# Optimization experiments

Measured on AMD Instinct MI355X. Metric: run time of the kernel, lower is better.

## Reference

```python
import jax, jax.numpy as jnp
import numpy as np

N_NODES = 50000
N_EDGES = 1600000
N_FEAT = 512
N_HID = 128
N_CLASSES = 2
NUM_GRAPHS = 128


def setup_inputs() -> dict:
    key = jax.random.key(0)
    k_x, k_e, k_w1, k_b1, k_w2, k_b2 = jax.random.split(key, 6)
    x = jax.random.normal(k_x, (N_NODES, N_FEAT), dtype=jnp.float32)
    edge_index = jax.random.randint(k_e, (2, N_EDGES), 0, N_NODES, dtype=jnp.int64)
    # evenly spaced graph ids -> every graph segment non-empty for max pool
    batch = (jnp.arange(N_NODES, dtype=jnp.int64) * NUM_GRAPHS) // N_NODES
    # GCNConv weight (glorot-ish) and bias; lin2 head
    W1 = jax.random.normal(k_w1, (N_FEAT, N_HID), dtype=jnp.float32) * (1.0 / np.sqrt(N_FEAT))
    b1 = jnp.zeros((N_HID,), dtype=jnp.float32)
    W2 = jax.random.normal(k_w2, (N_HID, N_CLASSES), dtype=jnp.float32) * (1.0 / np.sqrt(N_HID))
    b2 = jnp.zeros((N_CLASSES,), dtype=jnp.float32)
    return {"x": x, "W1": W1, "b1": b1, "W2": W2, "b2": b2,
            "edge_index": edge_index, "batch": batch}


def _gcn_conv(x, edge_index, W, b):
    # PyG GCNConv: add self loops, symmetric norm, aggregate src->dst
    src, dst = edge_index[0], edge_index[1]
    loops = jnp.arange(N_NODES, dtype=src.dtype)
    src = jnp.concatenate([src, loops])
    dst = jnp.concatenate([dst, loops])
    deg = jax.ops.segment_sum(jnp.ones_like(dst, dtype=x.dtype), dst,
                              num_segments=N_NODES)
    dinv = jnp.where(deg > 0, jax.lax.rsqrt(deg), 0.0)
    norm = dinv[src] * dinv[dst]                      # [E+N]
    h = x @ W                                         # [N, nhid]
    msgs = h[src] * norm[:, None]                     # gather + scale
    out = jax.ops.segment_sum(msgs, dst, num_segments=N_NODES)
    return out + b


def reference(x, W1, b1, W2, b2, edge_index, batch):
    h = jax.nn.relu(_gcn_conv(x, edge_index, W1, b1))       # [N, nhid]
    pooled = jax.ops.segment_max(h, batch, num_segments=NUM_GRAPHS)  # [G, nhid]
    logits = pooled @ W2 + b2                               # [G, num_classes]
    return jax.nn.log_softmax(logits, axis=-1)
```

## Files before the change

kernel.cpp:

```cpp
#include <hip/hip_runtime.h>

#define N_NODES   50000
#define N_EDGES   1600000
#define N_FEAT    512
#define N_HID     128
#define NUM_GRAPHS 128
#define N_WAVES_GEMM 3125
#define PREP_DINV_BLOCKS 196

#define CAP          96
#define NSLICE       8
#define SLICE_NODES  6250
#define NCHUNK       128
#define CHUNK_E      12500

typedef short bf16x8 __attribute__((ext_vector_type(8)));
typedef float f32x4  __attribute__((ext_vector_type(4)));

static __device__ __forceinline__ unsigned short f2bf(float f) {
  union { float f; unsigned int u; } v; v.f = f;
  unsigned int u = v.u;
  unsigned int r = (u + 0x7FFFu + ((u >> 16) & 1u)) >> 16;
  return (unsigned short)r;
}
static __device__ __forceinline__ float bfl(unsigned int w) {
  union { unsigned int u; float f; } v; v.u = w << 16; return v.f;
}
static __device__ __forceinline__ float bfh(unsigned int w) {
  union { unsigned int u; float f; } v; v.u = w & 0xFFFF0000u; return v.f;
}

__global__ void init_ws(int* __restrict__ cnt, int* __restrict__ pooled) {
  int i = blockIdx.x * 256 + threadIdx.x;
  if (i < N_NODES) cnt[i] = 0;
  if (i < NUM_GRAPHS * N_HID) pooled[i] = 0;
}

__global__ __launch_bounds__(256) void scatter_slice(const int* __restrict__ edge,
                                                     int* __restrict__ cnt,
                                                     unsigned short* __restrict__ sedge) {
  const int chunk = blockIdx.x >> 3;
  const int lo = (blockIdx.x & 7) * SLICE_NODES;
  const int e0 = chunk * CHUNK_E;
  for (int e = e0 + threadIdx.x; e < e0 + CHUNK_E; e += 256) {
    int d = edge[N_EDGES + e];
    if ((unsigned)(d - lo) < (unsigned)SLICE_NODES) {
      int s = edge[e];
      int pos = atomicAdd(&cnt[d], 1);
      if (pos < CAP) sedge[(size_t)d * CAP + pos] = (unsigned short)s;
    }
  }
}

__global__ __launch_bounds__(256) void prep(const int* __restrict__ cnt,
                                            float* __restrict__ dinv,
                                            unsigned short* __restrict__ sedge,
                                            unsigned short* __restrict__ h,
                                            const float* __restrict__ W,
                                            unsigned short* __restrict__ wT) {
  if (blockIdx.x < PREP_DINV_BLOCKS) {
    int node = blockIdx.x * 256 + threadIdx.x;
    if (node < N_NODES) {
      int c0 = cnt[node];
      dinv[node] = rsqrtf((float)(c0 + 1));
      int c = c0 > CAP ? CAP : c0;
      int p = (c + 7) & ~7; if (p > CAP) p = CAP;
      for (int k = c; k < p; k++)
        sedge[(size_t)node * CAP + k] = (unsigned short)N_NODES;
    }
    if (blockIdx.x == 0 && threadIdx.x < 64)
      ((unsigned int*)(h + (size_t)N_NODES * N_HID))[threadIdx.x] = 0u;
  } else {
    int i = (blockIdx.x - PREP_DINV_BLOCKS) * 256 + threadIdx.x;
    if (i < N_HID * N_FEAT) {
      int n = i >> 9, k = i & 511;
      wT[i] = f2bf(W[(size_t)k * N_HID + n]);
    }
  }
}

__global__ __launch_bounds__(256) void gemm_mfma(const float* __restrict__ x,
                                                 const unsigned short* __restrict__ wT,
                                                 const float* __restrict__ dinv,
                                                 unsigned short* __restrict__ h) {
  const int wave = (blockIdx.x * 256 + threadIdx.x) >> 6;
  if (wave >= N_WAVES_GEMM) return;
  const int lane = threadIdx.x & 63;
  const int row0 = wave * 16;
  const int arow = row0 + (lane & 15);
  const int kbase = (lane >> 4) * 8;

  f32x4 acc[8];
#pragma unroll
  for (int i = 0; i < 8; i++) acc[i] = (f32x4){0.f, 0.f, 0.f, 0.f};

  for (int k0 = 0; k0 < N_FEAT; k0 += 32) {
    const float* ap = x + (size_t)arow * N_FEAT + k0 + kbase;
    float4 a0 = *(const float4*)ap;
    float4 a1 = *(const float4*)(ap + 4);
    bf16x8 af;
    af[0] = (short)f2bf(a0.x); af[1] = (short)f2bf(a0.y);
    af[2] = (short)f2bf(a0.z); af[3] = (short)f2bf(a0.w);
    af[4] = (short)f2bf(a1.x); af[5] = (short)f2bf(a1.y);
    af[6] = (short)f2bf(a1.z); af[7] = (short)f2bf(a1.w);

#pragma unroll
    for (int ct = 0; ct < 8; ct++) {
      const bf16x8 bf = *(const bf16x8*)(wT + (size_t)(ct * 16 + (lane & 15)) * N_FEAT
                                            + k0 + kbase);
      acc[ct] = __builtin_amdgcn_mfma_f32_16x16x32_bf16(af, bf, acc[ct], 0, 0, 0);
    }
  }

  float dvv[4];
#pragma unroll
  for (int r = 0; r < 4; r++) dvv[r] = dinv[row0 + (lane >> 4) * 4 + r];
#pragma unroll
  for (int ct = 0; ct < 8; ct++) {
#pragma unroll
    for (int r = 0; r < 4; r++) {
      int row = row0 + (lane >> 4) * 4 + r;
      int col = ct * 16 + (lane & 15);
      h[(size_t)row * N_HID + col] = f2bf(acc[ct][r] * dvv[r]);
    }
  }
}

#define ACC8(V) { a0 += bfl((V).x); a1 += bfh((V).x); a2 += bfl((V).y); a3 += bfh((V).y); \
                  a4 += bfl((V).z); a5 += bfh((V).z); a6 += bfl((V).w); a7 += bfh((V).w); }
__global__ __launch_bounds__(512) void aggregate_pool(
    const unsigned short* __restrict__ h, const unsigned short* __restrict__ sedge,
    const float* __restrict__ dinv, const int* __restrict__ cnt,
    const float* __restrict__ b1, const int* __restrict__ batch,
    int* __restrict__ pooled) {
  __shared__ float vsh[8][128];
  __shared__ int gsh[8];
  const int wv = threadIdx.x >> 6;
  const int lane = threadIdx.x & 63;
  const int q = lane >> 4;
  const int fs8 = (lane & 15) * 8;
  const int node = blockIdx.x * 8 + wv;

  float a0 = 0.f, a1 = 0.f, a2 = 0.f, a3 = 0.f, a4 = 0.f, a5 = 0.f, a6 = 0.f, a7 = 0.f;

  if (q == 0) {
    uint4 w = *(const uint4*)(h + (size_t)node * N_HID + fs8);
    ACC8(w);
  }

  int c = cnt[node]; if (c > CAP) c = CAP;
  const int nv8 = ((c + 7) & ~7) >> 3;
  if (nv8 > 0) {
    const uint4* sv = (const uint4*)(sedge + (size_t)node * CAP);
    const int last = nv8 - 1;
    for (int vg = 0; vg < nv8; vg += 4) {
      int vidx = vg + q;
      uint4 ev = sv[vidx <= last ? vidx : last];
      bool ok = vidx <= last;
      int s0 = ok ? (int)(ev.x & 0xFFFFu) : N_NODES;
      int s1 = ok ? (int)(ev.x >> 16)     : N_NODES;
      int s2 = ok ? (int)(ev.y & 0xFFFFu) : N_NODES;
      int s3 = ok ? (int)(ev.y >> 16)     : N_NODES;
      int s4 = ok ? (int)(ev.z & 0xFFFFu) : N_NODES;
      int s5 = ok ? (int)(ev.z >> 16)     : N_NODES;
      int s6 = ok ? (int)(ev.w & 0xFFFFu) : N_NODES;
      int s7 = ok ? (int)(ev.w >> 16)     : N_NODES;
      uint4 w0 = *(const uint4*)(h + (size_t)s0 * N_HID + fs8);
      uint4 w1 = *(const uint4*)(h + (size_t)s1 * N_HID + fs8);
      uint4 w2 = *(const uint4*)(h + (size_t)s2 * N_HID + fs8);
      uint4 w3 = *(const uint4*)(h + (size_t)s3 * N_HID + fs8);
      uint4 w4 = *(const uint4*)(h + (size_t)s4 * N_HID + fs8);
      uint4 w5 = *(const uint4*)(h + (size_t)s5 * N_HID + fs8);
      uint4 w6 = *(const uint4*)(h + (size_t)s6 * N_HID + fs8);
      uint4 w7 = *(const uint4*)(h + (size_t)s7 * N_HID + fs8);
      ACC8(w0); ACC8(w1); ACC8(w2); ACC8(w3);
      ACC8(w4); ACC8(w5); ACC8(w6); ACC8(w7);
    }
  }

  a0 += __shfl_xor(a0, 16, 64); a1 += __shfl_xor(a1, 16, 64);
  a2 += __shfl_xor(a2, 16, 64); a3 += __shfl_xor(a3, 16, 64);
  a4 += __shfl_xor(a4, 16, 64); a5 += __shfl_xor(a5, 16, 64);
  a6 += __shfl_xor(a6, 16, 64); a7 += __shfl_xor(a7, 16, 64);
  a0 += __shfl_xor(a0, 32, 64); a1 += __shfl_xor(a1, 32, 64);
  a2 += __shfl_xor(a2, 32, 64); a3 += __shfl_xor(a3, 32, 64);
  a4 += __shfl_xor(a4, 32, 64); a5 += __shfl_xor(a5, 32, 64);
  a6 += __shfl_xor(a6, 32, 64); a7 += __shfl_xor(a7, 32, 64);

  const int g = batch[node];
  if (lane == 0) gsh[wv] = g;
  if (q == 0) {
    float dv = dinv[node];
    float4 ba = *(const float4*)(b1 + fs8);
    float4 bb = *(const float4*)(b1 + fs8 + 4);
    float4 v0, v1;
    v0.x = fmaxf(fmaf(a0, dv, ba.x), 0.f); v0.y = fmaxf(fmaf(a1, dv, ba.y), 0.f);
    v0.z = fmaxf(fmaf(a2, dv, ba.z), 0.f); v0.w = fmaxf(fmaf(a3, dv, ba.w), 0.f);
    v1.x = fmaxf(fmaf(a4, dv, bb.x), 0.f); v1.y = fmaxf(fmaf(a5, dv, bb.y), 0.f);
    v1.z = fmaxf(fmaf(a6, dv, bb.z), 0.f); v1.w = fmaxf(fmaf(a7, dv, bb.w), 0.f);
    *(float4*)(&vsh[wv][fs8]) = v0;
    *(float4*)(&vsh[wv][fs8 + 4]) = v1;
  }
  __syncthreads();
  int gprev = (wv > 0) ? gsh[wv - 1] : -1;
  if (g != gprev && q == 0) {
    float m[8];
#pragma unroll
    for (int j = 0; j < 8; j++) m[j] = vsh[wv][fs8 + j];
    for (int r = wv + 1; r < 8 && gsh[r] == g; r++)
#pragma unroll
      for (int j = 0; j < 8; j++) m[j] = fmaxf(m[j], vsh[r][fs8 + j]);
#pragma unroll
    for (int j = 0; j < 8; j++)
      atomicMax(&pooled[g * N_HID + fs8 + j], __float_as_int(m[j]));
  }
}

__global__ __launch_bounds__(128) void head_kernel(const int* __restrict__ pooled,
                                                   const float* __restrict__ W2,
                                                   const float* __restrict__ b2,
                                                   float* __restrict__ out) {
  __shared__ float sW[N_HID * 2];
  int t = threadIdx.x;
  sW[t] = W2[t];
  sW[t + 128] = W2[t + 128];
  __syncthreads();
  float l0 = b2[0], l1 = b2[1];
  for (int f = 0; f < N_HID; f++) {
    float pv = __int_as_float(pooled[t * N_HID + f]);
    l0 = fmaf(pv, sW[f * 2 + 0], l0);
    l1 = fmaf(pv, sW[f * 2 + 1], l1);
  }
  float m = fmaxf(l0, l1);
  float lse = m + logf(expf(l0 - m) + expf(l1 - m));
  out[t * 2 + 0] = l0 - lse;
  out[t * 2 + 1] = l1 - lse;
}

extern "C" void kernel_launch(void* const* d_in, const int* in_sizes, int n_in,
                              void* d_out, int out_size, void* d_ws, size_t ws_size,
                              hipStream_t stream) {
  const float* x   = (const float*)d_in[0];
  const float* W1  = (const float*)d_in[1];
  const float* b1  = (const float*)d_in[2];
  const float* W2  = (const float*)d_in[3];
  const float* b2  = (const float*)d_in[4];
  const int* edge  = (const int*)d_in[5];
  const int* batch = (const int*)d_in[6];
  float* out = (float*)d_out;

  char* ws = (char*)d_ws;
  int*   cnt    = (int*)(ws + 0);
  float* dinv   = (float*)(ws + 200704);
  int*   pooled = (int*)(ws + 401408);
  unsigned short* sedge = (unsigned short*)(ws + 466944);
  unsigned short* h  = (unsigned short*)(ws + 10066944);
  unsigned short* wT = (unsigned short*)(ws + 22867200);

  init_ws<<<196, 256, 0, stream>>>(cnt, pooled);
  scatter_slice<<<NCHUNK * NSLICE, 256, 0, stream>>>(edge, cnt, sedge);
  prep<<<PREP_DINV_BLOCKS + 256, 256, 0, stream>>>(cnt, dinv, sedge, h, W1, wT);
  gemm_mfma<<<(N_WAVES_GEMM + 3) / 4, 256, 0, stream>>>(x, wT, dinv, h);
  aggregate_pool<<<N_NODES / 8, 512, 0, stream>>>(h, sedge, dinv, cnt, b1, batch, pooled);
  head_kernel<<<1, 128, 0, stream>>>(pooled, W2, b2, out);
}
```

Baseline: 263.1 us.

## Co-schedule edge scatter with GEMM in one launch and apply dinv afterward

The edge-bucketing scatter and the bf16 MFMA GEMM now run in one launch with disjoint block ranges, so the atomic-bound scatter and the bandwidth-bound GEMM can overlap on the device. Because the GEMM no longer waits for the degree counts, dinv scaling moves into a new prep2 pass that rescales each h row in place and also pads the sedge lists. This pass adds an extra read and write of h and rounds to bf16 twice. The scatter also loads edges as int4, and the init kernel is replaced by hipMemsetAsync.

Result: slower. 270.5 us (+2.8%).

```diff
diff --git a/kernel.cpp b/kernel.cpp
--- a/kernel.cpp
+++ b/kernel.cpp
@@ -6,13 +6,14 @@
 #define N_HID     128
 #define NUM_GRAPHS 128
 #define N_WAVES_GEMM 3125
-#define PREP_DINV_BLOCKS 196
+#define GEMM_BLOCKS 782
 
 #define CAP          96
 #define NSLICE       8
 #define SLICE_NODES  6250
 #define NCHUNK       128
 #define CHUNK_E      12500
+#define SCAT_BLOCKS  (NCHUNK * NSLICE)
 
 typedef short bf16x8 __attribute__((ext_vector_type(8)));
 typedef float f32x4  __attribute__((ext_vector_type(4)));
@@ -30,100 +31,101 @@
   union { unsigned int u; float f; } v; v.u = w & 0xFFFF0000u; return v.f;
 }
 
-__global__ void init_ws(int* __restrict__ cnt, int* __restrict__ pooled) {
+__global__ __launch_bounds__(256) void wconv(const float* __restrict__ W,
+                                             unsigned short* __restrict__ wT) {
   int i = blockIdx.x * 256 + threadIdx.x;
-  if (i < N_NODES) cnt[i] = 0;
-  if (i < NUM_GRAPHS * N_HID) pooled[i] = 0;
-}
-
-__global__ __launch_bounds__(256) void scatter_slice(const int* __restrict__ edge,
-                                                     int* __restrict__ cnt,
-                                                     unsigned short* __restrict__ sedge) {
-  const int chunk = blockIdx.x >> 3;
-  const int lo = (blockIdx.x & 7) * SLICE_NODES;
-  const int e0 = chunk * CHUNK_E;
-  for (int e = e0 + threadIdx.x; e < e0 + CHUNK_E; e += 256) {
-    int d = edge[N_EDGES + e];
-    if ((unsigned)(d - lo) < (unsigned)SLICE_NODES) {
-      int s = edge[e];
-      int pos = atomicAdd(&cnt[d], 1);
-      if (pos < CAP) sedge[(size_t)d * CAP + pos] = (unsigned short)s;
-    }
-  }
-}
-
-__global__ __launch_bounds__(256) void prep(const int* __restrict__ cnt,
-                                            float* __restrict__ dinv,
-                                            unsigned short* __restrict__ sedge,
-                                            unsigned short* __restrict__ h,
-                                            const float* __restrict__ W,
-                                            unsigned short* __restrict__ wT) {
-  if (blockIdx.x < PREP_DINV_BLOCKS) {
-    int node = blockIdx.x * 256 + threadIdx.x;
-    if (node < N_NODES) {
-      int c0 = cnt[node];
-      dinv[node] = rsqrtf((float)(c0 + 1));
-      int c = c0 > CAP ? CAP : c0;
-      int p = (c + 7) & ~7; if (p > CAP) p = CAP;
-      for (int k = c; k < p; k++)
-        sedge[(size_t)node * CAP + k] = (unsigned short)N_NODES;
-    }
-    if (blockIdx.x == 0 && threadIdx.x < 64)
-      ((unsigned int*)(h + (size_t)N_NODES * N_HID))[threadIdx.x] = 0u;
+  if (i < N_HID * N_FEAT) {
+    int n = i >> 9, k = i & 511;
+    wT[i] = f2bf(W[(size_t)k * N_HID + n]);
+  }
+}
+
+__global__ __launch_bounds__(256) void gemm_scatter(const int* __restrict__ edge,
+                                                    int* __restrict__ cnt,
+                                                    unsigned short* __restrict__ sedge,
+                                                    const float* __restrict__ x,
+                                                    const unsigned short* __restrict__ wT,
+                                                    unsigned short* __restrict__ h) {
+  if (blockIdx.x < SCAT_BLOCKS) {
+    const int chunk = blockIdx.x >> 3;
+    const int lo = (blockIdx.x & 7) * SLICE_NODES;
+    const int e0 = chunk * CHUNK_E;
+    const int4* dstv = (const int4*)(edge + N_EDGES + e0);
+    const int4* srcv = (const int4*)(edge + e0);
+    for (int i = threadIdx.x; i < CHUNK_E / 4; i += 256) {
+      int4 d4 = dstv[i];
+      int4 s4 = srcv[i];
+#define SCAT1(D, S) if ((unsigned)((D) - lo) < (unsigned)SLICE_NODES) { \
+        int pos = atomicAdd(&cnt[D], 1); \
+        if (pos < CAP) sedge[(size_t)(D) * CAP + pos] = (unsigned short)(S); }
+      SCAT1(d4.x, s4.x); SCAT1(d4.y, s4.y); SCAT1(d4.z, s4.z); SCAT1(d4.w, s4.w);
+#undef SCAT1
+    }
   } else {
-    int i = (blockIdx.x - PREP_DINV_BLOCKS) * 256 + threadIdx.x;
-    if (i < N_HID * N_FEAT) {
-      int n = i >> 9, k = i & 511;
-      wT[i] = f2bf(W[(size_t)k * N_HID + n]);
-    }
-  }
-}
-
-__global__ __launch_bounds__(256) void gemm_mfma(const float* __restrict__ x,
-                                                 const unsigned short* __restrict__ wT,
-                                                 const float* __restrict__ dinv,
-                                                 unsigned short* __restrict__ h) {
-  const int wave = (blockIdx.x * 256 + threadIdx.x) >> 6;
-  if (wave >= N_WAVES_GEMM) return;
+    const int wave = ((blockIdx.x - SCAT_BLOCKS) * 256 + threadIdx.x) >> 6;
+    if (wave >= N_WAVES_GEMM) return;
+    const int lane = threadIdx.x & 63;
+    const int row0 = wave * 16;
+    const int arow = row0 + (lane & 15);
+    const int kbase = (lane >> 4) * 8;
+
+    f32x4 acc[8];
+#pragma unroll
+    for (int i = 0; i < 8; i++) acc[i] = (f32x4){0.f, 0.f, 0.f, 0.f};
+
+    for (int k0 = 0; k0 < N_FEAT; k0 += 32) {
+      const float* ap = x + (size_t)arow * N_FEAT + k0 + kbase;
+      float4 a0 = *(const float4*)ap;
+      float4 a1 = *(const float4*)(ap + 4);
+      bf16x8 af;
+      af[0] = (short)f2bf(a0.x); af[1] = (short)f2bf(a0.y);
+      af[2] = (short)f2bf(a0.z); af[3] = (short)f2bf(a0.w);
+      af[4] = (short)f2bf(a1.x); af[5] = (short)f2bf(a1.y);
+      af[6] = (short)f2bf(a1.z); af[7] = (short)f2bf(a1.w);
+
+#pragma unroll
+      for (int ct = 0; ct < 8; ct++) {
+        const bf16x8 bf = *(const bf16x8*)(wT + (size_t)(ct * 16 + (lane & 15)) * N_FEAT
+                                              + k0 + kbase);
+        acc[ct] = __builtin_amdgcn_mfma_f32_16x16x32_bf16(af, bf, acc[ct], 0, 0, 0);
+      }
+    }
+
+#pragma unroll
+    for (int ct = 0; ct < 8; ct++) {
+#pragma unroll
+      for (int r = 0; r < 4; r++) {
+        int row = row0 + (lane >> 4) * 4 + r;
+        int col = ct * 16 + (lane & 15);
+        h[(size_t)row * N_HID + col] = f2bf(acc[ct][r]);
+      }
+    }
+  }
+}
+
+__global__ __launch_bounds__(256) void prep2(const int* __restrict__ cnt,
+                                             float* __restrict__ dinv,
+                                             unsigned short* __restrict__ sedge,
+                                             unsigned short* __restrict__ h) {
+  const int row = (blockIdx.x * 256 + threadIdx.x) >> 6;
   const int lane = threadIdx.x & 63;
-  const int row0 = wave * 16;
-  const int arow = row0 + (lane & 15);
-  const int kbase = (lane >> 4) * 8;
-
-  f32x4 acc[8];
-#pragma unroll
-  for (int i = 0; i < 8; i++) acc[i] = (f32x4){0.f, 0.f, 0.f, 0.f};
-
-  for (int k0 = 0; k0 < N_FEAT; k0 += 32) {
-    const float* ap = x + (size_t)arow * N_FEAT + k0 + kbase;
-    float4 a0 = *(const float4*)ap;
-    float4 a1 = *(const float4*)(ap + 4);
-    bf16x8 af;
-    af[0] = (short)f2bf(a0.x); af[1] = (short)f2bf(a0.y);
-    af[2] = (short)f2bf(a0.z); af[3] = (short)f2bf(a0.w);
-    af[4] = (short)f2bf(a1.x); af[5] = (short)f2bf(a1.y);
-    af[6] = (short)f2bf(a1.z); af[7] = (short)f2bf(a1.w);
-
-#pragma unroll
-    for (int ct = 0; ct < 8; ct++) {
-      const bf16x8 bf = *(const bf16x8*)(wT + (size_t)(ct * 16 + (lane & 15)) * N_FEAT
-                                            + k0 + kbase);
-      acc[ct] = __builtin_amdgcn_mfma_f32_16x16x32_bf16(af, bf, acc[ct], 0, 0, 0);
-    }
-  }
-
-  float dvv[4];
-#pragma unroll
-  for (int r = 0; r < 4; r++) dvv[r] = dinv[row0 + (lane >> 4) * 4 + r];
-#pragma unroll
-  for (int ct = 0; ct < 8; ct++) {
-#pragma unroll
-    for (int r = 0; r < 4; r++) {
-      int row = row0 + (lane >> 4) * 4 + r;
-      int col = ct * 16 + (lane & 15);
-      h[(size_t)row * N_HID + col] = f2bf(acc[ct][r] * dvv[r]);
-    }
-  }
+  if (row > N_NODES) return;
+  unsigned int* hrow = (unsigned int*)(h + (size_t)row * N_HID);
+  if (row == N_NODES) { hrow[lane] = 0u; return; }
+
+  int c0 = cnt[row];
+  float dv = rsqrtf((float)(c0 + 1));
+  if (lane == 0) dinv[row] = dv;
+
+  unsigned int w = hrow[lane];
+  unsigned int lo16 = (unsigned int)f2bf(bfl(w) * dv);
+  unsigned int hi16 = (unsigned int)f2bf(bfh(w) * dv);
+  hrow[lane] = lo16 | (hi16 << 16);
+
+  int c = c0 > CAP ? CAP : c0;
+  int p = (c + 7) & ~7; if (p > CAP) p = CAP;
+  if (lane < p - c)
+    sedge[(size_t)row * CAP + c + lane] = (unsigned short)N_NODES;
 }
 
 #define ACC8(V) { a0 += bfl((V).x); a1 += bfh((V).x); a2 += bfl((V).y); a3 += bfh((V).y); \
@@ -257,10 +259,11 @@
   unsigned short* h  = (unsigned short*)(ws + 10066944);
   unsigned short* wT = (unsigned short*)(ws + 22867200);
 
-  init_ws<<<196, 256, 0, stream>>>(cnt, pooled);
-  scatter_slice<<<NCHUNK * NSLICE, 256, 0, stream>>>(edge, cnt, sedge);
-  prep<<<PREP_DINV_BLOCKS + 256, 256, 0, stream>>>(cnt, dinv, sedge, h, W1, wT);
-  gemm_mfma<<<(N_WAVES_GEMM + 3) / 4, 256, 0, stream>>>(x, wT, dinv, h);
+  hipMemsetAsync(cnt, 0, N_NODES * sizeof(int), stream);
+  hipMemsetAsync(pooled, 0, NUM_GRAPHS * N_HID * sizeof(int), stream);
+  wconv<<<(N_HID * N_FEAT + 255) / 256, 256, 0, stream>>>(W1, wT);
+  gemm_scatter<<<SCAT_BLOCKS + GEMM_BLOCKS, 256, 0, stream>>>(edge, cnt, sedge, x, wT, h);
+  prep2<<<(N_NODES + 4) / 4, 256, 0, stream>>>(cnt, dinv, sedge, h);
   aggregate_pool<<<N_NODES / 8, 512, 0, stream>>>(h, sedge, dinv, cnt, b1, batch, pooled);
   head_kernel<<<1, 128, 0, stream>>>(pooled, W2, b2, out);
 }
```

## Split aggregation across four feature quarters and vectorize edge scatter loads

Applied to the files above, without the earlier changes.

The aggregation kernel now launches four times as many blocks, and each block handles a 32-feature quarter of the hidden dimension with 4-byte gathers instead of 16-byte ones. The goal is better L2 locality of the gathered h slice and more parallelism. The cost is that the edge lists, cnt and dinv are re-read four times, and gathers become smaller and less efficient. The scatter kernel now reads src/dst as int4 vectors, and the init kernel is replaced by two hipMemsetAsync calls.

Measured after the change: 273.0 us. 3.7% more time.

```diff
diff --git a/kernel.cpp b/kernel.cpp
--- a/kernel.cpp
+++ b/kernel.cpp
@@ -13,6 +13,7 @@
 #define SLICE_NODES  6250
 #define NCHUNK       128
 #define CHUNK_E      12500
+#define AGG_GROUPS   6250
 
 typedef short bf16x8 __attribute__((ext_vector_type(8)));
 typedef float f32x4  __attribute__((ext_vector_type(4)));
@@ -28,12 +29,6 @@
 }
 static __device__ __forceinline__ float bfh(unsigned int w) {
   union { unsigned int u; float f; } v; v.u = w & 0xFFFF0000u; return v.f;
-}
-
-__global__ void init_ws(int* __restrict__ cnt, int* __restrict__ pooled) {
-  int i = blockIdx.x * 256 + threadIdx.x;
-  if (i < N_NODES) cnt[i] = 0;
-  if (i < NUM_GRAPHS * N_HID) pooled[i] = 0;
 }
 
 __global__ __launch_bounds__(256) void scatter_slice(const int* __restrict__ edge,
@@ -42,13 +37,16 @@
   const int chunk = blockIdx.x >> 3;
   const int lo = (blockIdx.x & 7) * SLICE_NODES;
   const int e0 = chunk * CHUNK_E;
-  for (int e = e0 + threadIdx.x; e < e0 + CHUNK_E; e += 256) {
-    int d = edge[N_EDGES + e];
-    if ((unsigned)(d - lo) < (unsigned)SLICE_NODES) {
-      int s = edge[e];
-      int pos = atomicAdd(&cnt[d], 1);
-      if (pos < CAP) sedge[(size_t)d * CAP + pos] = (unsigned short)s;
-    }
+  const int4* dstv = (const int4*)(edge + N_EDGES + e0);
+  const int4* srcv = (const int4*)(edge + e0);
+  for (int i = threadIdx.x; i < CHUNK_E / 4; i += 256) {
+    int4 d4 = dstv[i];
+    int4 s4 = srcv[i];
+#define SCAT1(D, S) if ((unsigned)((D) - lo) < (unsigned)SLICE_NODES) { \
+      int pos = atomicAdd(&cnt[D], 1); \
+      if (pos < CAP) sedge[(size_t)(D) * CAP + pos] = (unsigned short)(S); }
+    SCAT1(d4.x, s4.x); SCAT1(d4.y, s4.y); SCAT1(d4.z, s4.z); SCAT1(d4.w, s4.w);
+#undef SCAT1
   }
 }
 
@@ -126,26 +124,26 @@
   }
 }
 
-#define ACC8(V) { a0 += bfl((V).x); a1 += bfh((V).x); a2 += bfl((V).y); a3 += bfh((V).y); \
-                  a4 += bfl((V).z); a5 += bfh((V).z); a6 += bfl((V).w); a7 += bfh((V).w); }
-__global__ __launch_bounds__(512) void aggregate_pool(
+__global__ __launch_bounds__(512) void aggregate_q(
     const unsigned short* __restrict__ h, const unsigned short* __restrict__ sedge,
     const float* __restrict__ dinv, const int* __restrict__ cnt,
     const float* __restrict__ b1, const int* __restrict__ batch,
     int* __restrict__ pooled) {
-  __shared__ float vsh[8][128];
+  __shared__ float vsh[8][64];
   __shared__ int gsh[8];
+  const int qsel = blockIdx.x / AGG_GROUPS;
+  const int grp  = blockIdx.x % AGG_GROUPS;
+  const int fbase = qsel * 32;
   const int wv = threadIdx.x >> 6;
   const int lane = threadIdx.x & 63;
   const int q = lane >> 4;
-  const int fs8 = (lane & 15) * 8;
-  const int node = blockIdx.x * 8 + wv;
-
-  float a0 = 0.f, a1 = 0.f, a2 = 0.f, a3 = 0.f, a4 = 0.f, a5 = 0.f, a6 = 0.f, a7 = 0.f;
-
+  const int f2 = (lane & 15) * 2;
+  const int node = grp * 8 + wv;
+
+  float a0 = 0.f, a1 = 0.f;
   if (q == 0) {
-    uint4 w = *(const uint4*)(h + (size_t)node * N_HID + fs8);
-    ACC8(w);
+    unsigned int w = *(const unsigned int*)(h + (size_t)node * N_HID + fbase + f2);
+    a0 += bfl(w); a1 += bfh(w);
   }
 
   int c = cnt[node]; if (c > CAP) c = CAP;
@@ -165,54 +163,41 @@
       int s5 = ok ? (int)(ev.z >> 16)     : N_NODES;
       int s6 = ok ? (int)(ev.w & 0xFFFFu) : N_NODES;
       int s7 = ok ? (int)(ev.w >> 16)     : N_NODES;
-      uint4 w0 = *(const uint4*)(h + (size_t)s0 * N_HID + fs8);
-      uint4 w1 = *(const uint4*)(h + (size_t)s1 * N_HID + fs8);
-      uint4 w2 = *(const uint4*)(h + (size_t)s2 * N_HID + fs8);
-      uint4 w3 = *(const uint4*)(h + (size_t)s3 * N_HID + fs8);
-      uint4 w4 = *(const uint4*)(h + (size_t)s4 * N_HID + fs8);
-      uint4 w5 = *(const uint4*)(h + (size_t)s5 * N_HID + fs8);
-      uint4 w6 = *(const uint4*)(h + (size_t)s6 * N_HID + fs8);
-      uint4 w7 = *(const uint4*)(h + (size_t)s7 * N_HID + fs8);
-      ACC8(w0); ACC8(w1); ACC8(w2); ACC8(w3);
-      ACC8(w4); ACC8(w5); ACC8(w6); ACC8(w7);
+      unsigned int w0 = *(const unsigned int*)(h + (size_t)s0 * N_HID + fbase + f2);
+      unsigned int w1 = *(const unsigned int*)(h + (size_t)s1 * N_HID + fbase + f2);
+      unsigned int w2 = *(const unsigned int*)(h + (size_t)s2 * N_HID + fbase + f2);
+      unsigned int w3 = *(const unsigned int*)(h + (size_t)s3 * N_HID + fbase + f2);
+      unsigned int w4 = *(const unsigned int*)(h + (size_t)s4 * N_HID + fbase + f2);
+      unsigned int w5 = *(const unsigned int*)(h + (size_t)s5 * N_HID + fbase + f2);
+      unsigned int w6 = *(const unsigned int*)(h + (size_t)s6 * N_HID + fbase + f2);
+      unsigned int w7 = *(const unsigned int*)(h + (size_t)s7 * N_HID + fbase + f2);
+      a0 += bfl(w0); a1 += bfh(w0); a0 += bfl(w1); a1 += bfh(w1);
+      a0 += bfl(w2); a1 += bfh(w2); a0 += bfl(w3); a1 += bfh(w3);
+      a0 += bfl(w4); a1 += bfh(w4); a0 += bfl(w5); a1 += bfh(w5);
+      a0 += bfl(w6); a1 += bfh(w6); a0 += bfl(w7); a1 += bfh(w7);
     }
   }
 
   a0 += __shfl_xor(a0, 16, 64); a1 += __shfl_xor(a1, 16, 64);
-  a2 += __shfl_xor(a2, 16, 64); a3 += __shfl_xor(a3, 16, 64);
-  a4 += __shfl_xor(a4, 16, 64); a5 += __shfl_xor(a5, 16, 64);
-  a6 += __shfl_xor(a6, 16, 64); a7 += __shfl_xor(a7, 16, 64);
   a0 += __shfl_xor(a0, 32, 64); a1 += __shfl_xor(a1, 32, 64);
-  a2 += __shfl_xor(a2, 32, 64); a3 += __shfl_xor(a3, 32, 64);
-  a4 += __shfl_xor(a4, 32, 64); a5 += __shfl_xor(a5, 32, 64);
-  a6 += __shfl_xor(a6, 32, 64); a7 += __shfl_xor(a7, 32, 64);
 
   const int g = batch[node];
   if (lane == 0) gsh[wv] = g;
   if (q == 0) {
     float dv = dinv[node];
-    float4 ba = *(const float4*)(b1 + fs8);
-    float4 bb = *(const float4*)(b1 + fs8 + 4);
-    float4 v0, v1;
-    v0.x = fmaxf(fmaf(a0, dv, ba.x), 0.f); v0.y = fmaxf(fmaf(a1, dv, ba.y), 0.f);
-    v0.z = fmaxf(fmaf(a2, dv, ba.z), 0.f); v0.w = fmaxf(fmaf(a3, dv, ba.w), 0.f);
-    v1.x = fmaxf(fmaf(a4, dv, bb.x), 0.f); v1.y = fmaxf(fmaf(a5, dv, bb.y), 0.f);
-    v1.z = fmaxf(fmaf(a6, dv, bb.z), 0.f); v1.w = fmaxf(fmaf(a7, dv, bb.w), 0.f);
-    *(float4*)(&vsh[wv][fs8]) = v0;
-    *(float4*)(&vsh[wv][fs8 + 4]) = v1;
+    float v0 = fmaxf(fmaf(a0, dv, b1[fbase + f2]),     0.f);
+    float v1 = fmaxf(fmaf(a1, dv, b1[fbase + f2 + 1]), 0.f);
+    vsh[wv][f2] = v0; vsh[wv][f2 + 1] = v1;
   }
   __syncthreads();
   int gprev = (wv > 0) ? gsh[wv - 1] : -1;
   if (g != gprev && q == 0) {
-    float m[8];
-#pragma unroll
-    for (int j = 0; j < 8; j++) m[j] = vsh[wv][fs8 + j];
-    for (int r = wv + 1; r < 8 && gsh[r] == g; r++)
-#pragma unroll
-      for (int j = 0; j < 8; j++) m[j] = fmaxf(m[j], vsh[r][fs8 + j]);
-#pragma unroll
-    for (int j = 0; j < 8; j++)
-      atomicMax(&pooled[g * N_HID + fs8 + j], __float_as_int(m[j]));
+    float m0 = vsh[wv][f2], m1 = vsh[wv][f2 + 1];
+    for (int r = wv + 1; r < 8 && gsh[r] == g; r++) {
+      m0 = fmaxf(m0, vsh[r][f2]); m1 = fmaxf(m1, vsh[r][f2 + 1]);
+    }
+    atomicMax(&pooled[g * N_HID + fbase + f2],     __float_as_int(m0));
+    atomicMax(&pooled[g * N_HID + fbase + f2 + 1], __float_as_int(m1));
   }
 }
 
@@ -257,10 +242,11 @@
   unsigned short* h  = (unsigned short*)(ws + 10066944);
   unsigned short* wT = (unsigned short*)(ws + 22867200);
 
-  init_ws<<<196, 256, 0, stream>>>(cnt, pooled);
+  hipMemsetAsync(cnt, 0, N_NODES * sizeof(int), stream);
+  hipMemsetAsync(pooled, 0, NUM_GRAPHS * N_HID * sizeof(int), stream);
   scatter_slice<<<NCHUNK * NSLICE, 256, 0, stream>>>(edge, cnt, sedge);
   prep<<<PREP_DINV_BLOCKS + 256, 256, 0, stream>>>(cnt, dinv, sedge, h, W1, wT);
   gemm_mfma<<<(N_WAVES_GEMM + 3) / 4, 256, 0, stream>>>(x, wT, dinv, h);
-  aggregate_pool<<<N_NODES / 8, 512, 0, stream>>>(h, sedge, dinv, cnt, b1, batch, pooled);
+  aggregate_q<<<4 * AGG_GROUPS, 512, 0, stream>>>(h, sedge, dinv, cnt, b1, batch, pooled);
   head_kernel<<<1, 128, 0, stream>>>(pooled, W2, b2, out);
 }
```
